# Performance work log

Measured on AMD Instinct MI355X. Metric: run time of the kernel, lower is better.

The kernel has to match this reference:

```python
import jax, jax.numpy as jnp
import numpy as np

EMBED_DIM = 768
NUM_HEADS = 12
HEAD_DIM = EMBED_DIM // NUM_HEADS


def setup_inputs() -> dict:
    key = jax.random.key(0)
    k_x, k_wqkv, k_bqkv, k_wp, k_bp = jax.random.split(key, 5)
    B, N, C = 2, 2048, EMBED_DIM
    lim_qkv = 1.0 / np.sqrt(C)
    lim_p = 1.0 / np.sqrt(C)
    return {
        "x": jax.random.normal(k_x, (B, N, C), dtype=jnp.float32),
        # torch Linear weights: [out_features, in_features]
        "w_qkv": jax.random.uniform(k_wqkv, (3 * C, C), minval=-lim_qkv, maxval=lim_qkv, dtype=jnp.float32),
        "b_qkv": jax.random.uniform(k_bqkv, (3 * C,), minval=-lim_qkv, maxval=lim_qkv, dtype=jnp.float32),
        "w_proj": jax.random.uniform(k_wp, (C, C), minval=-lim_p, maxval=lim_p, dtype=jnp.float32),
        "b_proj": jax.random.uniform(k_bp, (C,), minval=-lim_p, maxval=lim_p, dtype=jnp.float32),
    }


def reference(x, w_qkv, b_qkv, w_proj, b_proj):
    b, n, c = x.shape
    h, d = NUM_HEADS, HEAD_DIM
    qkv = x @ w_qkv.T + b_qkv                      # [b, n, 3c]
    qkv = qkv.reshape(b, n, 3, h, d).transpose(2, 0, 3, 1, 4)  # [3, b, h, n, d]
    q, k, v = qkv[0], qkv[1], qkv[2]
    scale = d ** -0.5
    attn = jnp.einsum('bhnd,bhmd->bhnm', q, k) * scale  # [b, h, n, n]
    attn = jax.nn.softmax(attn, axis=-1)
    # dropout is identity at inference (eval mode)
    out = jnp.einsum('bhnm,bhmd->bhnd', attn, v)        # [b, h, n, d]
    out = out.transpose(0, 2, 1, 3).reshape(b, n, c)    # [b, n, c]
    return out @ w_proj.T + b_proj
```

## Files before the change

kernel.cpp:

```cpp
#include <hip/hip_runtime.h>
#include <cstdint>
#include <cstddef>

using u16    = uint16_t;
using u16x4  = __attribute__((ext_vector_type(4))) uint16_t;
using u16x8  = __attribute__((ext_vector_type(8))) uint16_t;
using bf16x2 = __attribute__((ext_vector_type(2))) __bf16;
using bf16x8 = __attribute__((ext_vector_type(8))) __bf16;
using f32x4  = __attribute__((ext_vector_type(4))) float;

__device__ __forceinline__ u16 f2b(float f) {
    union { float f; uint32_t u; } x; x.f = f;
    uint32_t r = x.u + 0x7FFFu + ((x.u >> 16) & 1u);
    return (u16)(r >> 16);
}
__device__ __forceinline__ uint32_t pk2(float a, float b) {
    bf16x2 t; t[0] = (__bf16)a; t[1] = (__bf16)b;
    return __builtin_bit_cast(uint32_t, t);
}
__device__ __forceinline__ bf16x8 ld8(const u16* p) {
    union { u16x8 v; u16x4 h[2]; } r;
    r.h[0] = *(const u16x4*)p;
    r.h[1] = *(const u16x4*)(p + 4);
    return __builtin_bit_cast(bf16x8, r.v);
}
__device__ __forceinline__ u16x8 ld8u(const u16* p) {
    union { u16x8 v; u16x4 h[2]; } r;
    r.h[0] = *(const u16x4*)p;
    r.h[1] = *(const u16x4*)(p + 4);
    return r.v;
}
__device__ __forceinline__ void st8(u16* p, u16x8 v) {
    union { u16x8 v; u16x4 h[2]; } r; r.v = v;
    *(u16x4*)p       = r.h[0];
    *(u16x4*)(p + 4) = r.h[1];
}

__device__ __forceinline__ void load16_async(const u16* g, u16* lds_base) {
    __builtin_amdgcn_global_load_lds(
        (const __attribute__((address_space(1))) u16*)g,
        (__attribute__((address_space(3))) u16*)(uint32_t)(uintptr_t)lds_base,
        16, 0, 0);
}

__global__ void conv_k(const float* __restrict__ x,  u16* __restrict__ xb,  int nx4,
                       const float* __restrict__ w1, u16* __restrict__ w1b, int n14,
                       const float* __restrict__ w2, u16* __restrict__ w2b, int n24)
{
    const int t   = blockIdx.x * blockDim.x + threadIdx.x;
    const int stp = gridDim.x * blockDim.x;
    for (int i = t; i < nx4; i += stp) {
        f32x4 v = ((const f32x4*)x)[i];
        u16x4 o;
        #pragma unroll
        for (int e = 0; e < 4; e++) o[e] = f2b(v[e]);
        ((u16x4*)xb)[i] = o;
    }
    for (int i = t; i < n14; i += stp) {
        f32x4 v = ((const f32x4*)w1)[i];
        u16x4 o;
        #pragma unroll
        for (int e = 0; e < 4; e++) o[e] = f2b(v[e]);
        ((u16x4*)w1b)[i] = o;
    }
    for (int i = t; i < n24; i += stp) {
        f32x4 v = ((const f32x4*)w2)[i];
        u16x4 o;
        #pragma unroll
        for (int e = 0; e < 4; e++) o[e] = f2b(v[e]);
        ((u16x4*)w2b)[i] = o;
    }
}

__global__ __launch_bounds__(256, 3) void gemm_qkv(
    const u16* __restrict__ A, const u16* __restrict__ W,
    const float* __restrict__ bias,
    u16* __restrict__ O0, u16* __restrict__ O1, u16* __restrict__ O2)
{
    __shared__ alignas(16) char smem[33792];
    u16* As = (u16*)smem;
    u16* Bs = (u16*)(smem + 8192);
    u16* T  = (u16*)smem;

    const int tid  = threadIdx.x;
    const int wid  = tid >> 6, lane = tid & 63;
    const int quad = lane >> 4, lc = lane & 15;
    const int row0 = blockIdx.x * 128, col0 = blockIdx.y * 128;
    const int wm   = (wid >> 1) * 64, wn = (wid & 1) * 64;

    const int srA = wid * 32 + (lane >> 2);
    const int scA = (lane & 3) * 8;

    f32x4 acc[4][4] = {};

    for (int k0 = 0; k0 < 768; k0 += 32) {
        __syncthreads();
        #pragma unroll
        for (int t = 0; t < 2; t++) {
            load16_async(&A[(row0 + srA + t*16) * 768 + k0 + scA], &As[wid*1024 + t*512]);
            load16_async(&W[(col0 + srA + t*16) * 768 + k0 + scA], &Bs[wid*1024 + t*512]);
        }
        __syncthreads();

        bf16x8 a[4], b[4];
        #pragma unroll
        for (int i = 0; i < 4; i++)
            a[i] = __builtin_bit_cast(bf16x8, *(const u16x8*)&As[(wm + i*16 + lc)*32 + quad*8]);
        #pragma unroll
        for (int j = 0; j < 4; j++)
            b[j] = __builtin_bit_cast(bf16x8, *(const u16x8*)&Bs[(wn + j*16 + lc)*32 + quad*8]);
        #pragma unroll
        for (int i = 0; i < 4; i++)
            #pragma unroll
            for (int j = 0; j < 4; j++)
                acc[i][j] = __builtin_amdgcn_mfma_f32_16x16x32_bf16(a[i], b[j], acc[i][j], 0, 0, 0);
    }

    if (col0 < 1536) {
        #pragma unroll
        for (int i = 0; i < 4; i++) {
            #pragma unroll
            for (int j = 0; j < 4; j++) {
                const int gc = col0 + wn + j*16 + lc;
                const float bv = bias[gc];
                #pragma unroll
                for (int r = 0; r < 4; r++) {
                    const int gr = row0 + wm + i*16 + quad*4 + r;
                    const u16 ob = f2b(acc[i][j][r] + bv);
                    if (gc < 768) O0[gr * 768 + gc] = ob;
                    else          O1[gr * 768 + (gc - 768)] = ob;
                }
            }
        }
    } else {
        __syncthreads();
        #pragma unroll
        for (int j = 0; j < 4; j++) {
            const int cl = wn + j*16 + lc;
            const float bv = bias[col0 + cl];
            #pragma unroll
            for (int i = 0; i < 4; i++) {
                uint2 w;
                w.x = pk2(acc[i][j][0] + bv, acc[i][j][1] + bv);
                w.y = pk2(acc[i][j][2] + bv, acc[i][j][3] + bv);
                *(uint2*)&T[cl*132 + wm + i*16 + quad*4] = w;
            }
        }
        __syncthreads();

        const int cl = tid >> 1;
        const int sg = (tid & 1) * 64;
        const int c2 = (col0 - 1536) + cl;
        const int hh = c2 >> 6, dd = c2 & 63;
        const int bb = row0 >> 11, nn0 = row0 & 2047;
        u16* dst = &O2[((size_t)((bb*12 + hh)*64 + dd))*2048 + nn0 + sg];
        #pragma unroll
        for (int k = 0; k < 8; k++)
            *(u16x8*)&dst[k*8] = ld8u(&T[cl*132 + sg + k*8]);
    }
}

__global__ __launch_bounds__(256, 4) void gemm_proj(
    const u16* __restrict__ A, const u16* __restrict__ W,
    const float* __restrict__ bias, float* __restrict__ F0)
{
    __shared__ alignas(16) u16 As[64 * 32];
    __shared__ alignas(16) u16 Bs[64 * 32];
    const int tid  = threadIdx.x;
    const int wid  = tid >> 6, lane = tid & 63;
    const int quad = lane >> 4, lc = lane & 15;
    const int row0 = blockIdx.x * 64, col0 = blockIdx.y * 64;
    const int wm   = (wid >> 1) * 32, wn = (wid & 1) * 32;

    const int srA = wid * 16 + (lane >> 2);
    const int scA = (lane & 3) * 8;

    f32x4 acc[2][2] = {};

    for (int k0 = 0; k0 < 768; k0 += 32) {
        __syncthreads();
        load16_async(&A[(row0 + srA) * 768 + k0 + scA], &As[wid*512]);
        load16_async(&W[(col0 + srA) * 768 + k0 + scA], &Bs[wid*512]);
        __syncthreads();

        bf16x8 a[2], b[2];
        #pragma unroll
        for (int i = 0; i < 2; i++)
            a[i] = __builtin_bit_cast(bf16x8, *(const u16x8*)&As[(wm + i*16 + lc)*32 + quad*8]);
        #pragma unroll
        for (int j = 0; j < 2; j++)
            b[j] = __builtin_bit_cast(bf16x8, *(const u16x8*)&Bs[(wn + j*16 + lc)*32 + quad*8]);
        #pragma unroll
        for (int i = 0; i < 2; i++)
            #pragma unroll
            for (int j = 0; j < 2; j++)
                acc[i][j] = __builtin_amdgcn_mfma_f32_16x16x32_bf16(a[i], b[j], acc[i][j], 0, 0, 0);
    }

    #pragma unroll
    for (int i = 0; i < 2; i++)
        #pragma unroll
        for (int j = 0; j < 2; j++) {
            const int gc = col0 + wn + j*16 + lc;
            const float bv = bias[gc];
            #pragma unroll
            for (int r = 0; r < 4; r++) {
                const int gr = row0 + wm + i*16 + quad*4 + r;
                F0[gr * 768 + gc] = acc[i][j][r] + bv;
            }
        }
}

__global__ __launch_bounds__(256, 2) void attn_k(
    const u16* __restrict__ Q, const u16* __restrict__ K,
    const u16* __restrict__ V, u16* __restrict__ O)
{
    __shared__ alignas(16) char lds[53760];
    u16* Ks = (u16*)(lds);
    u16* Vs = (u16*)(lds + 17408);
    u16* Ps = (u16*)(lds + 35328);
    float* Obuf = (float*)(lds);
    float* Lbuf = (float*)(lds + 35328);

    const int tid  = threadIdx.x;
    const int wid  = tid >> 6, lane = tid & 63;
    const int quad = lane >> 4, lc = lane & 15;
    const int li = blockIdx.x;
    const int bh = li >> 5, qt = li & 31;
    const int b = bh / 12, h = bh - b * 12;
    const int q0 = qt * 64;

    const u16* Qp = Q + ((size_t)b * 2048) * 768 + h * 64;
    const u16* Kp = K + ((size_t)b * 2048) * 768 + h * 64;
    const u16* Vp = V + (size_t)bh * 64 * 2048;
    u16*       Op = O + ((size_t)b * 2048) * 768 + h * 64;

    bf16x8 qf[4][2];
    #pragma unroll
    for (int qg = 0; qg < 4; qg++)
        #pragma unroll
        for (int kb = 0; kb < 2; kb++) {
            u16x8 t = *(const u16x8*)&Qp[(q0 + qg*16 + lc) * 768 + kb*32 + quad*8];
            bf16x8 sc;
            #pragma unroll
            for (int e = 0; e < 8; e++) {
                union { uint32_t u; float f; } z; z.u = ((uint32_t)t[e]) << 16;
                sc[e] = (__bf16)(z.f * 0.125f);
            }
            qf[qg][kb] = sc;
        }

    float l_[4] = {};
    f32x4 o_[4][4] = {};

    const int kr = tid >> 3, kseg = (tid & 7) * 8;
    const int vr = tid >> 4, vseg = (tid & 15) * 8;
    const int kb0 = wid * 32;

    u16x8 kpre[4], vpre[4];
    #pragma unroll
    for (int p = 0; p < 4; p++)
        kpre[p] = *(const u16x8*)&Kp[(kr + p*32)*768 + kseg];
    #pragma unroll
    for (int p = 0; p < 4; p++)
        vpre[p] = *(const u16x8*)&Vp[(vr + p*16)*2048 + vseg];

    for (int kt = 0; kt < 16; kt++) {
        __syncthreads();
        #pragma unroll
        for (int p = 0; p < 4; p++)
            st8(&Ks[(kr + p*32)*68 + kseg], kpre[p]);
        #pragma unroll
        for (int p = 0; p < 4; p++)
            st8(&Vs[(vr + p*16)*140 + vseg], vpre[p]);
        __syncthreads();

        if (kt < 15) {
            #pragma unroll
            for (int p = 0; p < 4; p++)
                kpre[p] = *(const u16x8*)&Kp[((kt+1)*128 + kr + p*32)*768 + kseg];
            #pragma unroll
            for (int p = 0; p < 4; p++)
                vpre[p] = *(const u16x8*)&Vp[(vr + p*16)*2048 + (kt+1)*128 + vseg];
        }

        f32x4 s[2][4] = {};
        __builtin_amdgcn_s_setprio(1);
        #pragma unroll
        for (int g = 0; g < 2; g++) {
            bf16x8 k0f = ld8(&Ks[(kb0 + g*16 + lc)*68 + quad*8]);
            bf16x8 k1f = ld8(&Ks[(kb0 + g*16 + lc)*68 + 32 + quad*8]);
            #pragma unroll
            for (int qg = 0; qg < 4; qg++) {
                s[g][qg] = __builtin_amdgcn_mfma_f32_16x16x32_bf16(k0f, qf[qg][0], s[g][qg], 0, 0, 0);
                s[g][qg] = __builtin_amdgcn_mfma_f32_16x16x32_bf16(k1f, qf[qg][1], s[g][qg], 0, 0, 0);
            }
        }
        __builtin_amdgcn_s_setprio(0);

        #pragma unroll
        for (int g = 0; g < 2; g++)
            #pragma unroll
            for (int qg = 0; qg < 4; qg++)
                #pragma unroll
                for (int r = 0; r < 4; r++) {
                    float p = __expf(s[g][qg][r]);
                    s[g][qg][r] = p;
                    l_[qg] += p;
                }

        #pragma unroll
        for (int g = 0; g < 2; g++)
            #pragma unroll
            for (int qg = 0; qg < 4; qg++) {
                uint2 w;
                w.x = pk2(s[g][qg][0], s[g][qg][1]);
                w.y = pk2(s[g][qg][2], s[g][qg][3]);
                *(uint2*)&Ps[(wid*64 + qg*16 + lc)*36 + g*16 + quad*4] = w;
            }

        bf16x8 pf[4], vf[4];
        #pragma unroll
        for (int qg = 0; qg < 4; qg++)
            pf[qg] = ld8(&Ps[(wid*64 + qg*16 + lc)*36 + quad*8]);
        #pragma unroll
        for (int dg = 0; dg < 4; dg++)
            vf[dg] = ld8(&Vs[(dg*16 + lc)*140 + kb0 + quad*8]);
        __builtin_amdgcn_s_setprio(1);
        #pragma unroll
        for (int dg = 0; dg < 4; dg++)
            #pragma unroll
            for (int qg = 0; qg < 4; qg++)
                o_[dg][qg] = __builtin_amdgcn_mfma_f32_16x16x32_bf16(vf[dg], pf[qg], o_[dg][qg], 0, 0, 0);
        __builtin_amdgcn_s_setprio(0);
    }

    #pragma unroll
    for (int qg = 0; qg < 4; qg++) {
        l_[qg] += __shfl_xor(l_[qg], 16);
        l_[qg] += __shfl_xor(l_[qg], 32);
    }
    __syncthreads();
    if (quad == 0)
        #pragma unroll
        for (int qg = 0; qg < 4; qg++)
            Lbuf[wid*64 + qg*16 + lc] = l_[qg];
    __syncthreads();

    const int eq = tid & 63;
    const int ed = (tid >> 6) * 8;
    const float linv = 1.0f / (Lbuf[0*64 + eq] + Lbuf[1*64 + eq] +
                               Lbuf[2*64 + eq] + Lbuf[3*64 + eq]);

    #pragma unroll
    for (int dh = 0; dh < 2; dh++) {
        __syncthreads();
        #pragma unroll
        for (int b2 = 0; b2 < 2; b2++) {
            const int dg = dh*2 + b2;
            #pragma unroll
            for (int qg = 0; qg < 4; qg++)
                #pragma unroll
                for (int r = 0; r < 4; r++)
                    Obuf[(wid*32 + b2*16 + quad*4 + r)*64 + qg*16 + lc] = o_[dg][qg][r];
        }
        __syncthreads();
        u16x8 ov;
        #pragma unroll
        for (int j = 0; j < 8; j++) {
            const float sum = Obuf[(0*32 + ed + j)*64 + eq] + Obuf[(1*32 + ed + j)*64 + eq] +
                              Obuf[(2*32 + ed + j)*64 + eq] + Obuf[(3*32 + ed + j)*64 + eq];
            ov[j] = f2b(sum * linv);
        }
        *(u16x8*)&Op[(size_t)(q0 + eq) * 768 + dh*32 + ed] = ov;
    }
}

extern "C" void kernel_launch(void* const* d_in, const int* in_sizes, int n_in,
                              void* d_out, int out_size, void* d_ws, size_t ws_size,
                              hipStream_t stream)
{
    const float* x    = (const float*)d_in[0];
    const float* wqkv = (const float*)d_in[1];
    const float* bqkv = (const float*)d_in[2];
    const float* wp   = (const float*)d_in[3];
    const float* bp   = (const float*)d_in[4];
    float* out = (float*)d_out;
    char* ws = (char*)d_ws;

    u16* Qw    = (u16*)(ws);
    u16* Vt    = (u16*)(ws + 6291456);
    u16* wqkvb = (u16*)(ws + 12582912);
    u16* wpb   = (u16*)(ws + 16121856);
    u16* Kw    = (u16*)d_out;
    u16* xb    = (u16*)((char*)d_out + 6291456);

    conv_k<<<512, 256, 0, stream>>>(x, xb, 3145728/4, wqkv, wqkvb, 1769472/4, wp, wpb, 589824/4);
    gemm_qkv<<<dim3(32, 18), 256, 0, stream>>>(xb, wqkvb, bqkv, Qw, Kw, Vt);
    attn_k<<<768, 256, 0, stream>>>(Qw, Kw, Vt, Qw);
    gemm_proj<<<dim3(64, 12), 256, 0, stream>>>(Qw, wpb, bp, out);
}
```

Before: 161.0 us.

## Split PV accumulation across wave pairs to halve O accumulators and raise occupancy

The PV product is repartitioned so each wave owns only half the head dimension (32 columns) over two key sub-blocks read from the shared P buffer, instead of all 64 columns over its own keys. This halves the per-wave output accumulator registers and raises the launch-bounds occupancy target from 2 to 3 blocks per CU. In exchange it adds an extra block-wide barrier per key tile before the PV stage. The epilogue is simplified to a single padded Obuf write and a reduction over two partials, which drops the two-pass loop.

```diff
diff --git a/kernel.cpp b/kernel.cpp
--- a/kernel.cpp
+++ b/kernel.cpp
@@ -211,7 +211,7 @@
         }
 }
 
-__global__ __launch_bounds__(256, 2) void attn_k(
+__global__ __launch_bounds__(256, 3) void attn_k(
     const u16* __restrict__ Q, const u16* __restrict__ K,
     const u16* __restrict__ V, u16* __restrict__ O)
 {
@@ -251,11 +251,13 @@
         }
 
     float l_[4] = {};
-    f32x4 o_[4][4] = {};
+    f32x4 o_[2][4] = {};
 
     const int kr = tid >> 3, kseg = (tid & 7) * 8;
     const int vr = tid >> 4, vseg = (tid & 15) * 8;
-    const int kb0 = wid * 32;
+    const int kb0   = wid * 32;
+    const int kh    = wid >> 1;
+    const int dbase = (wid & 1) * 32;
 
     u16x8 kpre[4], vpre[4];
     #pragma unroll
@@ -319,20 +321,26 @@
                 *(uint2*)&Ps[(wid*64 + qg*16 + lc)*36 + g*16 + quad*4] = w;
             }
 
-        bf16x8 pf[4], vf[4];
-        #pragma unroll
-        for (int qg = 0; qg < 4; qg++)
-            pf[qg] = ld8(&Ps[(wid*64 + qg*16 + lc)*36 + quad*8]);
-        #pragma unroll
-        for (int dg = 0; dg < 4; dg++)
-            vf[dg] = ld8(&Vs[(dg*16 + lc)*140 + kb0 + quad*8]);
-        __builtin_amdgcn_s_setprio(1);
-        #pragma unroll
-        for (int dg = 0; dg < 4; dg++)
+        __syncthreads();
+
+        #pragma unroll
+        for (int kb = 0; kb < 2; kb++) {
+            const int pw = kh*2 + kb;
+            bf16x8 pf[4], vf[2];
             #pragma unroll
             for (int qg = 0; qg < 4; qg++)
-                o_[dg][qg] = __builtin_amdgcn_mfma_f32_16x16x32_bf16(vf[dg], pf[qg], o_[dg][qg], 0, 0, 0);
-        __builtin_amdgcn_s_setprio(0);
+                pf[qg] = ld8(&Ps[(pw*64 + qg*16 + lc)*36 + quad*8]);
+            #pragma unroll
+            for (int dg = 0; dg < 2; dg++)
+                vf[dg] = ld8(&Vs[(dbase + dg*16 + lc)*140 + kh*64 + kb*32 + quad*8]);
+            __builtin_amdgcn_s_setprio(1);
+            #pragma unroll
+            for (int dg = 0; dg < 2; dg++)
+                #pragma unroll
+                for (int qg = 0; qg < 4; qg++)
+                    o_[dg][qg] = __builtin_amdgcn_mfma_f32_16x16x32_bf16(vf[dg], pf[qg], o_[dg][qg], 0, 0, 0);
+            __builtin_amdgcn_s_setprio(0);
+        }
     }
 
     #pragma unroll
@@ -345,35 +353,37 @@
         #pragma unroll
         for (int qg = 0; qg < 4; qg++)
             Lbuf[wid*64 + qg*16 + lc] = l_[qg];
+
+    #pragma unroll
+    for (int dg = 0; dg < 2; dg++)
+        #pragma unroll
+        for (int qg = 0; qg < 4; qg++)
+            #pragma unroll
+            for (int r = 0; r < 4; r++)
+                Obuf[(wid*32 + dg*16 + quad*4 + r)*65 + qg*16 + lc] = o_[dg][qg][r];
     __syncthreads();
 
     const int eq = tid & 63;
-    const int ed = (tid >> 6) * 8;
+    const int es = tid >> 6;
     const float linv = 1.0f / (Lbuf[0*64 + eq] + Lbuf[1*64 + eq] +
                                Lbuf[2*64 + eq] + Lbuf[3*64 + eq]);
-
-    #pragma unroll
-    for (int dh = 0; dh < 2; dh++) {
-        __syncthreads();
-        #pragma unroll
-        for (int b2 = 0; b2 < 2; b2++) {
-            const int dg = dh*2 + b2;
-            #pragma unroll
-            for (int qg = 0; qg < 4; qg++)
-                #pragma unroll
-                for (int r = 0; r < 4; r++)
-                    Obuf[(wid*32 + b2*16 + quad*4 + r)*64 + qg*16 + lc] = o_[dg][qg][r];
-        }
-        __syncthreads();
-        u16x8 ov;
-        #pragma unroll
-        for (int j = 0; j < 8; j++) {
-            const float sum = Obuf[(0*32 + ed + j)*64 + eq] + Obuf[(1*32 + ed + j)*64 + eq] +
-                              Obuf[(2*32 + ed + j)*64 + eq] + Obuf[(3*32 + ed + j)*64 + eq];
-            ov[j] = f2b(sum * linv);
-        }
-        *(u16x8*)&Op[(size_t)(q0 + eq) * 768 + dh*32 + ed] = ov;
-    }
+    const int dh = es >> 1;
+    const int dl = (es & 1) * 16;
+    const int r0 = dh * 32 * 65, r1 = (dh + 2) * 32 * 65;
+
+    u16x8 ov0, ov1;
+    #pragma unroll
+    for (int j = 0; j < 8; j++) {
+        const float sum = Obuf[r0 + (dl + j)*65 + eq] + Obuf[r1 + (dl + j)*65 + eq];
+        ov0[j] = f2b(sum * linv);
+    }
+    #pragma unroll
+    for (int j = 0; j < 8; j++) {
+        const float sum = Obuf[r0 + (dl + 8 + j)*65 + eq] + Obuf[r1 + (dl + 8 + j)*65 + eq];
+        ov1[j] = f2b(sum * linv);
+    }
+    *(u16x8*)&Op[(size_t)(q0 + eq) * 768 + es*16]     = ov0;
+    *(u16x8*)&Op[(size_t)(q0 + eq) * 768 + es*16 + 8] = ov1;
 }
 
 extern "C" void kernel_launch(void* const* d_in, const int* in_sizes, int n_in,
```

New measurement: 156.4 us. 1.03x faster.
